# Kernel tuning notes

Hardware: AMD Instinct MI355X
Metric: run time of the kernel (lower is better)

## Reference

```python
import jax, jax.numpy as jnp
import numpy as np

# physics constants (match PDELoss defaults)
RHO, CP, VZ, KT = 0.3, 1200.0, 0.5, 0.06
# Arrhenius-style soot source constants (representative RadiationPINN.soot_source_terms)
A_NUC, E_NUC = 1.0e4, 2.0e4
A_GROW, E_GROW = 5.0e3, 1.2e4
A_OX, E_OX = 1.0e5, 1.6e4

N, IN_DIM, H, OUT, N_FUELS, EMB = 262144, 12, 128, 7, 4, 8


def mlp(X, emb_rows, W1, b1, W2, b2, W3, b3, Wo, bo):
    # X: (N,4) coords; emb_rows: (N,8) fuel embedding -> T (N,1), fv (N,1), Y (N,5)
    h = jnp.concatenate([X, emb_rows], axis=-1)
    h = jnp.tanh(h @ W1 + b1)
    h = jnp.tanh(h @ W2 + b2)
    h = jnp.tanh(h @ W3 + b3)
    o = h @ Wo + bo
    T = 300.0 + 2000.0 * jax.nn.sigmoid(o[:, 0:1])
    fv = jax.nn.softplus(o[:, 1:2]) * 1e-6
    Y = jax.nn.softmax(o[:, 2:7], axis=-1)
    return T, fv, Y


def soot_sources(T, Y_prec, Y_O2, fv):
    nuc = A_NUC * Y_prec * jnp.exp(-E_NUC / T)
    grow = A_GROW * Y_prec * fv * jnp.exp(-E_GROW / T)
    ox = A_OX * Y_O2 * fv * jnp.sqrt(T) * jnp.exp(-E_OX / T)
    return nuc, grow, ox


def pde_loss(inputs, fuel_ids, W1, b1, W2, b2, W3, b3, Wo, bo, emb):
    emb_rows = emb[fuel_ids]  # (N, EMB), constant w.r.t. inputs
    params = (W1, b1, W2, b2, W3, b3, Wo, bo)

    def T_of(X):
        return mlp(X, emb_rows, *params)[0]

    def fv_of(X):
        return mlp(X, emb_rows, *params)[1]

    n = inputs.shape[0]
    Ez = jnp.zeros_like(inputs).at[:, 1].set(1.0)  # direction d/dz
    Er = jnp.zeros_like(inputs).at[:, 2].set(1.0)  # direction d/dr

    # forward-mode (Taylor) derivatives: nested jvp gives 1st and 2nd order in one pass
    dT_dz_fn = lambda X: jax.jvp(T_of, (X,), (Ez,))[1]
    dT_dz, d2T_dz2 = jax.jvp(dT_dz_fn, (inputs,), (Ez,))
    dT_dr_fn = lambda X: jax.jvp(T_of, (X,), (Er,))[1]
    dT_dr, d2T_dr2 = jax.jvp(dT_dr_fn, (inputs,), (Er,))
    _, dfv_dz = jax.jvp(fv_of, (inputs,), (Ez,))

    T, fv, Y = mlp(inputs, emb_rows, *params)
    Y_prec, Y_O2 = Y[:, 3:4], Y[:, 4:5]

    r = inputs[:, 2:3]
    r_safe = jnp.maximum(r, 1e-6)
    laplacian_r = d2T_dr2 + dT_dr / r_safe
    energy_res = RHO * CP * VZ * dT_dz - KT * laplacian_r - KT * d2T_dz2

    nuc, grow, ox = soot_sources(T, Y_prec, Y_O2, fv)
    soot_res = VZ * dfv_dz - nuc - grow + ox

    loss_energy = jnp.mean(energy_res ** 2)
    loss_soot = jnp.mean(soot_res ** 2)
    return jnp.stack([loss_energy, loss_soot, loss_energy + loss_soot])


def setup_inputs() -> dict:
    key = jax.random.key(0)
    ks = jax.random.split(key, 12)
    inputs = jax.random.uniform(ks[0], (N, 4), dtype=jnp.float32)
    fuel_ids = jax.random.randint(ks[1], (N,), 0, N_FUELS)
    s1, sh, so = 1.0 / np.sqrt(IN_DIM), 1.0 / np.sqrt(H), 1.0 / np.sqrt(H)
    return {
        "inputs": inputs,
        "fuel_ids": fuel_ids,
        "W1": jax.random.normal(ks[2], (IN_DIM, H), jnp.float32) * s1,
        "b1": jnp.zeros((H,), jnp.float32),
        "W2": jax.random.normal(ks[3], (H, H), jnp.float32) * sh,
        "b2": jnp.zeros((H,), jnp.float32),
        "W3": jax.random.normal(ks[4], (H, H), jnp.float32) * sh,
        "b3": jnp.zeros((H,), jnp.float32),
        "Wo": jax.random.normal(ks[5], (H, OUT), jnp.float32) * so,
        "bo": jnp.zeros((OUT,), jnp.float32),
        "emb": jax.random.normal(ks[6], (N_FUELS, EMB), jnp.float32) * 0.1,
    }


def reference(inputs, fuel_ids, W1, b1, W2, b2, W3, b3, Wo, bo, emb):
    return pde_loss(inputs, fuel_ids, W1, b1, W2, b2, W3, b3, Wo, bo, emb)
```

## Files before the change

### kernel.cpp

```cpp
#include <hip/hip_runtime.h>
#include <math.h>

#define NPTS 262144
#define PTS  16
#define NBLK (NPTS / PTS)

typedef _Float16 f16;
typedef f16    f16x4 __attribute__((ext_vector_type(4)));
typedef f16    f16x8 __attribute__((ext_vector_type(8)));
typedef __fp16 h16x2 __attribute__((ext_vector_type(2)));
typedef __fp16 h16x4 __attribute__((ext_vector_type(4)));
typedef float  f32x4 __attribute__((ext_vector_type(4)));
typedef int    i32x4 __attribute__((ext_vector_type(4)));


__device__ __forceinline__ h16x2 pk(float a, float b) {
    return __builtin_amdgcn_cvt_pkrtz(a, b);
}
__device__ __forceinline__ f16x4 mrg(h16x2 lo, h16x2 hi) {
    h16x4 v = __builtin_shufflevector(lo, hi, 0, 1, 2, 3);
    return __builtin_bit_cast(f16x4, v);
}
__device__ __forceinline__ int bc(h16x2 v) {
    return __builtin_bit_cast(int, v);
}
__device__ __forceinline__ void pin(f16x8& x) {
    asm volatile("" : "+v"(x));
}

__device__ __forceinline__ float fast_tanh(float z) {
    float e = __expf(2.f * z);
    float r = __builtin_amdgcn_rcpf(e + 1.f);
    return __builtin_fmaf(-2.f, r, 1.f);
}

__global__ void prep_weights(const float* __restrict__ W1, const float* __restrict__ W2,
                             const float* __restrict__ W3, const float* __restrict__ Wo,
                             const float* __restrict__ bo,
                             f16* __restrict__ wt1, f16* __restrict__ wt2,
                             f16* __restrict__ wt3, f16* __restrict__ wot,
                             float* __restrict__ bot)
{
    int tid    = blockIdx.x * blockDim.x + threadIdx.x;
    int stride = gridDim.x * blockDim.x;
    for (int i = tid; i < 128 * 32; i += stride) {
        int k = i >> 7, n = i & 127;
        wt1[n * 32 + k] = (f16)((k < 12) ? W1[k * 128 + n] : 0.f);
    }
    for (int i = tid; i < 128 * 128; i += stride) {
        int k = i >> 7, n = i & 127;
        wt2[n * 128 + k] = (f16)W2[i];
        wt3[n * 128 + k] = (f16)W3[i];
    }
    for (int i = tid; i < 16 * 128; i += stride) {
        int k = i >> 4, n = i & 15;
        wot[n * 128 + k] = (f16)((n < 7) ? Wo[k * 7 + n] : 0.f);
    }
    if (tid < 16) bot[tid] = (tid < 7) ? bo[tid] : 0.f;
}

__device__ __forceinline__ void transform_store(
    char* sA, const f32x4 acc[5], int pt, int n0q)
{
    float t[4], s[4];
#pragma unroll
    for (int r = 0; r < 4; ++r) {
        t[r] = fast_tanh(acc[0][r]);
        s[r] = 1.f - t[r] * t[r];
    }
    h16x2 T[2]  = { pk(t[0], t[1]), pk(t[2], t[3]) };
    h16x2 S[2]  = { pk(s[0], s[1]), pk(s[2], s[3]) };
    h16x2 A1[2] = { pk(acc[1][0], acc[1][1]), pk(acc[1][2], acc[1][3]) };
    h16x2 A2[2] = { pk(acc[2][0], acc[2][1]), pk(acc[2][2], acc[2][3]) };
    h16x2 A3[2] = { pk(acc[3][0], acc[3][1]), pk(acc[3][2], acc[3][3]) };
    h16x2 A4[2] = { pk(acc[4][0], acc[4][1]), pk(acc[4][2], acc[4][3]) };
    h16x2 TZ[2], TZZ[2], TR[2], TRR[2];
#pragma unroll
    for (int p = 0; p < 2; ++p) {
        h16x2 n2t = -(T[p] + T[p]);
        TZ[p]  = S[p] * A1[p];
        TR[p]  = S[p] * A3[p];
        TZZ[p] = n2t * (TZ[p] * A1[p]) + S[p] * A2[p];
        TRR[p] = n2t * (TR[p] * A3[p]) + S[p] * A4[p];
    }
    const int key = (pt & 7) << 4;
    char* rb = sA + (pt << 8) + (((n0q * 2)) ^ key);
    *(f16x4*)(rb)         = mrg(T[0], T[1]);
    *(f16x4*)(rb +  4096) = mrg(TZ[0], TZ[1]);
    *(f16x4*)(rb +  8192) = mrg(TZZ[0], TZZ[1]);
    *(f16x4*)(rb + 12288) = mrg(TR[0], TR[1]);
    *(f16x4*)(rb + 16384) = mrg(TRR[0], TRR[1]);
}

__device__ __forceinline__ void transform_store_l1(
    char* sA, const f32x4 acc0, const f32x4 wz, const f32x4 wr,
    int pt, int n0q)
{
    float t[4], s[4];
#pragma unroll
    for (int r = 0; r < 4; ++r) {
        t[r] = fast_tanh(acc0[r]);
        s[r] = 1.f - t[r] * t[r];
    }
    h16x2 T[2]  = { pk(t[0], t[1]), pk(t[2], t[3]) };
    h16x2 S[2]  = { pk(s[0], s[1]), pk(s[2], s[3]) };
    h16x2 A1[2] = { pk(wz[0], wz[1]), pk(wz[2], wz[3]) };
    h16x2 A3[2] = { pk(wr[0], wr[1]), pk(wr[2], wr[3]) };
    h16x2 TZ[2], TZZ[2], TR[2], TRR[2];
#pragma unroll
    for (int p = 0; p < 2; ++p) {
        h16x2 n2t = -(T[p] + T[p]);
        TZ[p]  = S[p] * A1[p];
        TR[p]  = S[p] * A3[p];
        TZZ[p] = n2t * (TZ[p] * A1[p]);
        TRR[p] = n2t * (TR[p] * A3[p]);
    }
    const int key = (pt & 7) << 4;
    char* rb = sA + (pt << 8) + (((n0q * 2)) ^ key);
    *(f16x4*)(rb)         = mrg(T[0], T[1]);
    *(f16x4*)(rb +  4096) = mrg(TZ[0], TZ[1]);
    *(f16x4*)(rb +  8192) = mrg(TZZ[0], TZZ[1]);
    *(f16x4*)(rb + 12288) = mrg(TR[0], TR[1]);
    *(f16x4*)(rb + 16384) = mrg(TRR[0], TRR[1]);
}

__device__ __forceinline__ void layer128(
    char* sA, const f16* __restrict__ Wt, const float* __restrict__ b,
    int q, int m)
{
    const int mkey = (m & 7) << 4;
    const char* rp = sA + (m << 8);
    f16x8 Bv[5][4];
#pragma unroll
    for (int c = 0; c < 5; ++c)
#pragma unroll
        for (int kt = 0; kt < 4; ++kt) {
            Bv[c][kt] = *(const f16x8*)(rp + c * 4096 + ((kt * 64 + q * 16) ^ mkey));
            pin(Bv[c][kt]);
        }

    const f32x4 z4 = {0.f, 0.f, 0.f, 0.f};
#pragma unroll
    for (int ct0 = 0; ct0 < 8; ++ct0) {
        const int n0 = ct0 * 16;
        const f16* wp = &Wt[(n0 + m) * 128 + q * 8];
        f16x8 A0 = *(const f16x8*)(wp);
        f16x8 A1 = *(const f16x8*)(wp + 32);
        f16x8 A2 = *(const f16x8*)(wp + 64);
        f16x8 A3 = *(const f16x8*)(wp + 96);
        f32x4 bb = *(const f32x4*)&b[n0 + q * 4];
        f32x4 acc[5];
        acc[0] = __builtin_amdgcn_mfma_f32_16x16x32_f16(A0, Bv[0][0], bb, 0, 0, 0);
#pragma unroll
        for (int c = 1; c < 5; ++c) acc[c] = __builtin_amdgcn_mfma_f32_16x16x32_f16(A0, Bv[c][0], z4, 0, 0, 0);
#pragma unroll
        for (int c = 0; c < 5; ++c) acc[c] = __builtin_amdgcn_mfma_f32_16x16x32_f16(A1, Bv[c][1], acc[c], 0, 0, 0);
#pragma unroll
        for (int c = 0; c < 5; ++c) acc[c] = __builtin_amdgcn_mfma_f32_16x16x32_f16(A2, Bv[c][2], acc[c], 0, 0, 0);
#pragma unroll
        for (int c = 0; c < 5; ++c) acc[c] = __builtin_amdgcn_mfma_f32_16x16x32_f16(A3, Bv[c][3], acc[c], 0, 0, 0);

        transform_store(sA, acc, m, n0 + q * 4);
    }
}

__global__ __launch_bounds__(64, 2) void pde_main(
    const float* __restrict__ X,
    const int*   __restrict__ fid,
    const float* __restrict__ emb,
    const float* __restrict__ W1,
    const float* __restrict__ b1, const float* __restrict__ b2,
    const float* __restrict__ b3,
    const f16* __restrict__ Wt1, const f16* __restrict__ Wt2,
    const f16* __restrict__ Wt3, const f16* __restrict__ Wot,
    const float* __restrict__ bot,
    float* __restrict__ partials)
{
    __shared__ f32x4 smem4[1280];
    char* sA = (char*)smem4;

    const int lane = threadIdx.x;
    const int q    = lane >> 4;
    const int m    = lane & 15;
    const int p0   = blockIdx.x * PTS;

    float rcoord = 0.f;
    if (lane < PTS) {
        const int p = lane;
        f32x4 xr = *(const f32x4*)&X[(p0 + p) * 4];
        rcoord = xr.z;
        const float* er = &emb[fid[p0 + p] * 8];
        f32x4 e0 = *(const f32x4*)er;
        f32x4 e1 = *(const f32x4*)(er + 4);
        const int key = (p & 7) << 4;
        char* rb = sA + (p << 8);
        i32x4 w0 = { bc(pk(xr.x, xr.y)), bc(pk(xr.z, xr.w)),
                     bc(pk(e0.x, e0.y)), bc(pk(e0.z, e0.w)) };
        i32x4 w1 = { bc(pk(e1.x, e1.y)), bc(pk(e1.z, e1.w)), 0, 0 };
        const i32x4 z16 = {0, 0, 0, 0};
        *(i32x4*)(rb + (0  ^ key)) = w0;
        *(i32x4*)(rb + (16 ^ key)) = w1;
        *(i32x4*)(rb + (32 ^ key)) = z16;
        *(i32x4*)(rb + (48 ^ key)) = z16;
    }

    {
        const int mkey = (m & 7) << 4;
        f16x8 Bv0 = *(const f16x8*)(sA + (m << 8) + ((q * 16) ^ mkey));
        pin(Bv0);
#pragma unroll
        for (int ct0 = 0; ct0 < 8; ++ct0) {
            const int n0 = ct0 * 16;
            f16x8 A0 = *(const f16x8*)&Wt1[(n0 + m) * 32 + q * 8];
            f32x4 bb = *(const f32x4*)&b1[n0 + q * 4];
            f32x4 acc0 = __builtin_amdgcn_mfma_f32_16x16x32_f16(A0, Bv0, bb, 0, 0, 0);
            f32x4 wz = *(const f32x4*)&W1[128 + n0 + q * 4];
            f32x4 wr = *(const f32x4*)&W1[256 + n0 + q * 4];
            transform_store_l1(sA, acc0, wz, wr, m, n0 + q * 4);
        }
    }

    layer128(sA, Wt2, b2, q, m);
    layer128(sA, Wt3, b3, q, m);

    f32x4 acc[5];
    {
        const int mkey = (m & 7) << 4;
        const char* rp = sA + (m << 8);
        f16x8 Bh[5][4];
#pragma unroll
        for (int c = 0; c < 5; ++c)
#pragma unroll
            for (int kt = 0; kt < 4; ++kt)
                Bh[c][kt] = *(const f16x8*)(rp + c * 4096 + ((kt * 64 + q * 16) ^ mkey));
        f32x4 c0i = *(const f32x4*)&bot[q * 4];
        const f16* wp = &Wot[m * 128 + q * 8];
        f16x8 A0 = *(const f16x8*)(wp);
        f16x8 A1 = *(const f16x8*)(wp + 32);
        f16x8 A2 = *(const f16x8*)(wp + 64);
        f16x8 A3 = *(const f16x8*)(wp + 96);
        const f32x4 z4 = {0.f, 0.f, 0.f, 0.f};
        acc[0] = __builtin_amdgcn_mfma_f32_16x16x32_f16(A0, Bh[0][0], c0i, 0, 0, 0);
#pragma unroll
        for (int c = 1; c < 5; ++c) acc[c] = __builtin_amdgcn_mfma_f32_16x16x32_f16(A0, Bh[c][0], z4, 0, 0, 0);
#pragma unroll
        for (int c = 0; c < 5; ++c) acc[c] = __builtin_amdgcn_mfma_f32_16x16x32_f16(A1, Bh[c][1], acc[c], 0, 0, 0);
#pragma unroll
        for (int c = 0; c < 5; ++c) acc[c] = __builtin_amdgcn_mfma_f32_16x16x32_f16(A2, Bh[c][2], acc[c], 0, 0, 0);
#pragma unroll
        for (int c = 0; c < 5; ++c) acc[c] = __builtin_amdgcn_mfma_f32_16x16x32_f16(A3, Bh[c][3], acc[c], 0, 0, 0);
    }
    const int src = (lane & 15) + 16;
    float o4 = __shfl(acc[0][0], src, 64);
    float o5 = __shfl(acc[0][1], src, 64);
    float o6 = __shfl(acc[0][2], src, 64);

    if (lane < PTS) {
        float o0   = acc[0][0], o1  = acc[0][1];
        float o0z  = acc[1][0], o1z = acc[1][1];
        float o0zz = acc[2][0];
        float o0r  = acc[3][0];
        float o0rr = acc[4][0];

        float sg  = __fdividef(1.f, 1.f + __expf(-o0));
        float T   = 300.f + 2000.f * sg;
        float sp  = sg * (1.f - sg);
        float spp = sp * (1.f - 2.f * sg);
        float Tz  = 2000.f * sp * o0z;
        float Tzz = 2000.f * (spp * o0z * o0z + sp * o0zz);
        float Tr  = 2000.f * sp * o0r;
        float Trr = 2000.f * (spp * o0r * o0r + sp * o0rr);

        float rs  = fmaxf(rcoord, 1e-6f);
        float lap = Trr + __fdividef(Tr, rs);
        float eres = 180.f * Tz - 0.06f * lap - 0.06f * Tzz;

        float fv  = ((o1 > 20.f) ? o1 : __logf(1.f + __expf(o1))) * 1e-6f;
        float s1  = __fdividef(1.f, 1.f + __expf(-o1));
        float fvz = s1 * o1z * 1e-6f;

        float y0 = acc[0][2], y1 = acc[0][3], y2 = o4, y3 = o5, y4 = o6;
        float mx = fmaxf(fmaxf(fmaxf(y0, y1), fmaxf(y2, y3)), y4);
        float e0 = __expf(y0 - mx), e1 = __expf(y1 - mx), e2 = __expf(y2 - mx);
        float e3 = __expf(y3 - mx), e4 = __expf(y4 - mx);
        float inv = __fdividef(1.f, e0 + e1 + e2 + e3 + e4);
        float Yp = e3 * inv;
        float Yo = e4 * inv;

        float rT  = __fdividef(1.f, T);
        float nuc  = 1e4f * Yp * __expf(-20000.f * rT);
        float grow = 5e3f * Yp * fv * __expf(-12000.f * rT);
        float ox   = 1e5f * Yo * fv * sqrtf(T) * __expf(-16000.f * rT);
        float sres = 0.5f * fvz - nuc - grow + ox;

        float ve = eres * eres;
        float vs = sres * sres;
#pragma unroll
        for (int o = 8; o > 0; o >>= 1) {
            ve += __shfl_xor(ve, o, 64);
            vs += __shfl_xor(vs, o, 64);
        }
        if (lane == 0) {
            float2 w; w.x = ve; w.y = vs;
            *(float2*)&partials[2 * blockIdx.x] = w;
        }
    }
}

__global__ __launch_bounds__(1024) void pde_finalize(
    const float* __restrict__ partials, float* __restrict__ out)
{
    __shared__ double rE[1024];
    __shared__ double rS[1024];
    const int tid = threadIdx.x;
    const float2* p2 = (const float2*)partials;
    double se = 0.0, ss = 0.0;
    for (int i = tid; i < NBLK; i += 1024) {
        float2 v = p2[i];
        se += (double)v.x;
        ss += (double)v.y;
    }
    rE[tid] = se; rS[tid] = ss;
    __syncthreads();
    for (int s = 512; s > 0; s >>= 1) {
        if (tid < s) { rE[tid] += rE[tid + s]; rS[tid] += rS[tid + s]; }
        __syncthreads();
    }
    if (tid == 0) {
        const double invN = 1.0 / (double)NPTS;
        float le = (float)(rE[0] * invN);
        float ls = (float)(rS[0] * invN);
        out[0] = le;
        out[1] = ls;
        out[2] = le + ls;
    }
}

extern "C" void kernel_launch(void* const* d_in, const int* in_sizes, int n_in,
                              void* d_out, int out_size, void* d_ws, size_t ws_size,
                              hipStream_t stream)
{
    const float* X   = (const float*)d_in[0];
    const int*   fid = (const int*)  d_in[1];
    const float* W1  = (const float*)d_in[2];
    const float* b1  = (const float*)d_in[3];
    const float* W2  = (const float*)d_in[4];
    const float* b2  = (const float*)d_in[5];
    const float* W3  = (const float*)d_in[6];
    const float* b3  = (const float*)d_in[7];
    const float* Wo  = (const float*)d_in[8];
    const float* bo  = (const float*)d_in[9];
    const float* emb = (const float*)d_in[10];

    f16*   wt1      = (f16*)d_ws;
    f16*   wt2      = wt1 + 128 * 32;
    f16*   wt3      = wt2 + 128 * 128;
    f16*   wot      = wt3 + 128 * 128;
    float* bot      = (float*)(wot + 16 * 128);
    float* partials = bot + 16;
    float* out      = (float*)d_out;

    prep_weights<<<128, 256, 0, stream>>>(W1, W2, W3, Wo, bo, wt1, wt2, wt3, wot, bot);
    pde_main<<<NBLK, 64, 0, stream>>>(X, fid, emb, W1, b1, b2, b3,
                                      wt1, wt2, wt3, wot, bot, partials);
    pde_finalize<<<1, 1024, 0, stream>>>(partials, out);
}
```

Baseline: 239.2 us.

## Keep second-derivative activations in registers via cross-lane shuffle transpose instead of LDS

The TZZ and TRR activation channels are no longer written to shared memory. They are carried in registers and rearranged into the MFMA B-operand layout with wave shuffles (xpose_pair), pairing column tiles. This shrinks LDS from 20KB to 12KB and raises the launch bound to 3 waves per SIMD, to improve occupancy and cut LDS traffic. In exchange it adds many ds_bpermute shuffles and more live registers, which may cause spills under the tighter register budget.

```diff
diff --git a/kernel.cpp b/kernel.cpp
--- a/kernel.cpp
+++ b/kernel.cpp
@@ -24,14 +24,29 @@
 __device__ __forceinline__ int bc(h16x2 v) {
     return __builtin_bit_cast(int, v);
 }
-__device__ __forceinline__ void pin(f16x8& x) {
-    asm volatile("" : "+v"(x));
+__device__ __forceinline__ f16x8 asf16(i32x4 v) {
+    return __builtin_bit_cast(f16x8, v);
 }
 
 __device__ __forceinline__ float fast_tanh(float z) {
     float e = __expf(2.f * z);
     float r = __builtin_amdgcn_rcpf(e + 1.f);
     return __builtin_fmaf(-2.f, r, 1.f);
+}
+
+__device__ __forceinline__ i32x4 xpose_pair(int E0, int E1, int O0, int O1,
+                                            int s0, int s1, int hi)
+{
+    int e0 = __shfl(E0, s0, 64), o0 = __shfl(O0, s0, 64);
+    int e1 = __shfl(E1, s0, 64), o1 = __shfl(O1, s0, 64);
+    int e2 = __shfl(E0, s1, 64), o2 = __shfl(O0, s1, 64);
+    int e3 = __shfl(E1, s1, 64), o3 = __shfl(O1, s1, 64);
+    i32x4 d;
+    d.x = hi ? o0 : e0;
+    d.y = hi ? o1 : e1;
+    d.z = hi ? o2 : e2;
+    d.w = hi ? o3 : e3;
+    return d;
 }
 
 __global__ void prep_weights(const float* __restrict__ W1, const float* __restrict__ W2,
@@ -59,8 +74,9 @@
     if (tid < 16) bot[tid] = (tid < 7) ? bo[tid] : 0.f;
 }
 
-__device__ __forceinline__ void transform_store(
-    char* sA, const f32x4 acc[5], int pt, int n0q)
+__device__ __forceinline__ void transform_store3(
+    char* sA, const f32x4 acc[5], int pt, int n0q,
+    int& zz0, int& zz1, int& rr0, int& rr1)
 {
     float t[4], s[4];
 #pragma unroll
@@ -85,16 +101,16 @@
     }
     const int key = (pt & 7) << 4;
     char* rb = sA + (pt << 8) + (((n0q * 2)) ^ key);
-    *(f16x4*)(rb)         = mrg(T[0], T[1]);
-    *(f16x4*)(rb +  4096) = mrg(TZ[0], TZ[1]);
-    *(f16x4*)(rb +  8192) = mrg(TZZ[0], TZZ[1]);
-    *(f16x4*)(rb + 12288) = mrg(TR[0], TR[1]);
-    *(f16x4*)(rb + 16384) = mrg(TRR[0], TRR[1]);
-}
-
-__device__ __forceinline__ void transform_store_l1(
+    *(f16x4*)(rb)        = mrg(T[0], T[1]);
+    *(f16x4*)(rb + 4096) = mrg(TZ[0], TZ[1]);
+    *(f16x4*)(rb + 8192) = mrg(TR[0], TR[1]);
+    zz0 = bc(TZZ[0]); zz1 = bc(TZZ[1]);
+    rr0 = bc(TRR[0]); rr1 = bc(TRR[1]);
+}
+
+__device__ __forceinline__ void transform_store3_l1(
     char* sA, const f32x4 acc0, const f32x4 wz, const f32x4 wr,
-    int pt, int n0q)
+    int pt, int n0q, int& zz0, int& zz1, int& rr0, int& rr1)
 {
     float t[4], s[4];
 #pragma unroll
@@ -117,54 +133,78 @@
     }
     const int key = (pt & 7) << 4;
     char* rb = sA + (pt << 8) + (((n0q * 2)) ^ key);
-    *(f16x4*)(rb)         = mrg(T[0], T[1]);
-    *(f16x4*)(rb +  4096) = mrg(TZ[0], TZ[1]);
-    *(f16x4*)(rb +  8192) = mrg(TZZ[0], TZZ[1]);
-    *(f16x4*)(rb + 12288) = mrg(TR[0], TR[1]);
-    *(f16x4*)(rb + 16384) = mrg(TRR[0], TRR[1]);
+    *(f16x4*)(rb)        = mrg(T[0], T[1]);
+    *(f16x4*)(rb + 4096) = mrg(TZ[0], TZ[1]);
+    *(f16x4*)(rb + 8192) = mrg(TR[0], TR[1]);
+    zz0 = bc(TZZ[0]); zz1 = bc(TZZ[1]);
+    rr0 = bc(TRR[0]); rr1 = bc(TRR[1]);
 }
 
 __device__ __forceinline__ void layer128(
     char* sA, const f16* __restrict__ Wt, const float* __restrict__ b,
-    int q, int m)
+    int q, int m, int s0, int s1, int hi,
+    const i32x4* Bzz_in, const i32x4* Brr_in,
+    i32x4* Bzz_out, i32x4* Brr_out)
 {
     const int mkey = (m & 7) << 4;
     const char* rp = sA + (m << 8);
-    f16x8 Bv[5][4];
-#pragma unroll
-    for (int c = 0; c < 5; ++c)
-#pragma unroll
-        for (int kt = 0; kt < 4; ++kt) {
+    f16x8 Bv[3][4];
+#pragma unroll
+    for (int c = 0; c < 3; ++c)
+#pragma unroll
+        for (int kt = 0; kt < 4; ++kt)
             Bv[c][kt] = *(const f16x8*)(rp + c * 4096 + ((kt * 64 + q * 16) ^ mkey));
-            pin(Bv[c][kt]);
+
+    const f32x4 z4 = {0.f, 0.f, 0.f, 0.f};
+#pragma unroll
+    for (int pr = 0; pr < 4; ++pr) {
+        int zE0, zE1, rE0, rE1, zO0, zO1, rO0, rO1;
+#pragma unroll
+        for (int half = 0; half < 2; ++half) {
+            const int ct0 = pr * 2 + half;
+            const int n0 = ct0 * 16;
+            const f16* wp = &Wt[(n0 + m) * 128 + q * 8];
+            f16x8 A0 = *(const f16x8*)(wp);
+            f16x8 A1 = *(const f16x8*)(wp + 32);
+            f16x8 A2 = *(const f16x8*)(wp + 64);
+            f16x8 A3 = *(const f16x8*)(wp + 96);
+            f32x4 bb = *(const f32x4*)&b[n0 + q * 4];
+            f32x4 acc[5];
+            acc[0] = __builtin_amdgcn_mfma_f32_16x16x32_f16(A0, Bv[0][0], bb, 0, 0, 0);
+            acc[1] = __builtin_amdgcn_mfma_f32_16x16x32_f16(A0, Bv[1][0], z4, 0, 0, 0);
+            acc[2] = __builtin_amdgcn_mfma_f32_16x16x32_f16(A0, asf16(Bzz_in[0]), z4, 0, 0, 0);
+            acc[3] = __builtin_amdgcn_mfma_f32_16x16x32_f16(A0, Bv[2][0], z4, 0, 0, 0);
+            acc[4] = __builtin_amdgcn_mfma_f32_16x16x32_f16(A0, asf16(Brr_in[0]), z4, 0, 0, 0);
+
+            acc[0] = __builtin_amdgcn_mfma_f32_16x16x32_f16(A1, Bv[0][1], acc[0], 0, 0, 0);
+            acc[1] = __builtin_amdgcn_mfma_f32_16x16x32_f16(A1, Bv[1][1], acc[1], 0, 0, 0);
+            acc[2] = __builtin_amdgcn_mfma_f32_16x16x32_f16(A1, asf16(Bzz_in[1]), acc[2], 0, 0, 0);
+            acc[3] = __builtin_amdgcn_mfma_f32_16x16x32_f16(A1, Bv[2][1], acc[3], 0, 0, 0);
+            acc[4] = __builtin_amdgcn_mfma_f32_16x16x32_f16(A1, asf16(Brr_in[1]), acc[4], 0, 0, 0);
+
+            acc[0] = __builtin_amdgcn_mfma_f32_16x16x32_f16(A2, Bv[0][2], acc[0], 0, 0, 0);
+            acc[1] = __builtin_amdgcn_mfma_f32_16x16x32_f16(A2, Bv[1][2], acc[1], 0, 0, 0);
+            acc[2] = __builtin_amdgcn_mfma_f32_16x16x32_f16(A2, asf16(Bzz_in[2]), acc[2], 0, 0, 0);
+            acc[3] = __builtin_amdgcn_mfma_f32_16x16x32_f16(A2, Bv[2][2], acc[3], 0, 0, 0);
+            acc[4] = __builtin_amdgcn_mfma_f32_16x16x32_f16(A2, asf16(Brr_in[2]), acc[4], 0, 0, 0);
+
+            acc[0] = __builtin_amdgcn_mfma_f32_16x16x32_f16(A3, Bv[0][3], acc[0], 0, 0, 0);
+            acc[1] = __builtin_amdgcn_mfma_f32_16x16x32_f16(A3, Bv[1][3], acc[1], 0, 0, 0);
+            acc[2] = __builtin_amdgcn_mfma_f32_16x16x32_f16(A3, asf16(Bzz_in[3]), acc[2], 0, 0, 0);
+            acc[3] = __builtin_amdgcn_mfma_f32_16x16x32_f16(A3, Bv[2][3], acc[3], 0, 0, 0);
+            acc[4] = __builtin_amdgcn_mfma_f32_16x16x32_f16(A3, asf16(Brr_in[3]), acc[4], 0, 0, 0);
+
+            int z0, z1, r0, r1;
+            transform_store3(sA, acc, m, n0 + q * 4, z0, z1, r0, r1);
+            if (half == 0) { zE0 = z0; zE1 = z1; rE0 = r0; rE1 = r1; }
+            else           { zO0 = z0; zO1 = z1; rO0 = r0; rO1 = r1; }
         }
-
-    const f32x4 z4 = {0.f, 0.f, 0.f, 0.f};
-#pragma unroll
-    for (int ct0 = 0; ct0 < 8; ++ct0) {
-        const int n0 = ct0 * 16;
-        const f16* wp = &Wt[(n0 + m) * 128 + q * 8];
-        f16x8 A0 = *(const f16x8*)(wp);
-        f16x8 A1 = *(const f16x8*)(wp + 32);
-        f16x8 A2 = *(const f16x8*)(wp + 64);
-        f16x8 A3 = *(const f16x8*)(wp + 96);
-        f32x4 bb = *(const f32x4*)&b[n0 + q * 4];
-        f32x4 acc[5];
-        acc[0] = __builtin_amdgcn_mfma_f32_16x16x32_f16(A0, Bv[0][0], bb, 0, 0, 0);
-#pragma unroll
-        for (int c = 1; c < 5; ++c) acc[c] = __builtin_amdgcn_mfma_f32_16x16x32_f16(A0, Bv[c][0], z4, 0, 0, 0);
-#pragma unroll
-        for (int c = 0; c < 5; ++c) acc[c] = __builtin_amdgcn_mfma_f32_16x16x32_f16(A1, Bv[c][1], acc[c], 0, 0, 0);
-#pragma unroll
-        for (int c = 0; c < 5; ++c) acc[c] = __builtin_amdgcn_mfma_f32_16x16x32_f16(A2, Bv[c][2], acc[c], 0, 0, 0);
-#pragma unroll
-        for (int c = 0; c < 5; ++c) acc[c] = __builtin_amdgcn_mfma_f32_16x16x32_f16(A3, Bv[c][3], acc[c], 0, 0, 0);
-
-        transform_store(sA, acc, m, n0 + q * 4);
-    }
-}
-
-__global__ __launch_bounds__(64, 2) void pde_main(
+        Bzz_out[pr] = xpose_pair(zE0, zE1, zO0, zO1, s0, s1, hi);
+        Brr_out[pr] = xpose_pair(rE0, rE1, rO0, rO1, s0, s1, hi);
+    }
+}
+
+__global__ __launch_bounds__(64, 3) void pde_main(
     const float* __restrict__ X,
     const int*   __restrict__ fid,
     const float* __restrict__ emb,
@@ -176,13 +216,16 @@
     const float* __restrict__ bot,
     float* __restrict__ partials)
 {
-    __shared__ f32x4 smem4[1280];
+    __shared__ f32x4 smem4[768];
     char* sA = (char*)smem4;
 
     const int lane = threadIdx.x;
     const int q    = lane >> 4;
     const int m    = lane & 15;
     const int p0   = blockIdx.x * PTS;
+    const int s0   = ((q & 1) << 5) + m;
+    const int s1   = s0 + 16;
+    const int hi   = q >> 1;
 
     float rcoord = 0.f;
     if (lane < PTS) {
@@ -204,32 +247,43 @@
         *(i32x4*)(rb + (48 ^ key)) = z16;
     }
 
+    i32x4 BzzA[4], BrrA[4], BzzB[4], BrrB[4];
+
     {
         const int mkey = (m & 7) << 4;
         f16x8 Bv0 = *(const f16x8*)(sA + (m << 8) + ((q * 16) ^ mkey));
-        pin(Bv0);
-#pragma unroll
-        for (int ct0 = 0; ct0 < 8; ++ct0) {
-            const int n0 = ct0 * 16;
-            f16x8 A0 = *(const f16x8*)&Wt1[(n0 + m) * 32 + q * 8];
-            f32x4 bb = *(const f32x4*)&b1[n0 + q * 4];
-            f32x4 acc0 = __builtin_amdgcn_mfma_f32_16x16x32_f16(A0, Bv0, bb, 0, 0, 0);
-            f32x4 wz = *(const f32x4*)&W1[128 + n0 + q * 4];
-            f32x4 wr = *(const f32x4*)&W1[256 + n0 + q * 4];
-            transform_store_l1(sA, acc0, wz, wr, m, n0 + q * 4);
+#pragma unroll
+        for (int pr = 0; pr < 4; ++pr) {
+            int zE0, zE1, rE0, rE1, zO0, zO1, rO0, rO1;
+#pragma unroll
+            for (int half = 0; half < 2; ++half) {
+                const int ct0 = pr * 2 + half;
+                const int n0 = ct0 * 16;
+                f16x8 A0 = *(const f16x8*)&Wt1[(n0 + m) * 32 + q * 8];
+                f32x4 bb = *(const f32x4*)&b1[n0 + q * 4];
+                f32x4 acc0 = __builtin_amdgcn_mfma_f32_16x16x32_f16(A0, Bv0, bb, 0, 0, 0);
+                f32x4 wz = *(const f32x4*)&W1[128 + n0 + q * 4];
+                f32x4 wr = *(const f32x4*)&W1[256 + n0 + q * 4];
+                int z0, z1, r0, r1;
+                transform_store3_l1(sA, acc0, wz, wr, m, n0 + q * 4, z0, z1, r0, r1);
+                if (half == 0) { zE0 = z0; zE1 = z1; rE0 = r0; rE1 = r1; }
+                else           { zO0 = z0; zO1 = z1; rO0 = r0; rO1 = r1; }
+            }
+            BzzA[pr] = xpose_pair(zE0, zE1, zO0, zO1, s0, s1, hi);
+            BrrA[pr] = xpose_pair(rE0, rE1, rO0, rO1, s0, s1, hi);
         }
     }
 
-    layer128(sA, Wt2, b2, q, m);
-    layer128(sA, Wt3, b3, q, m);
+    layer128(sA, Wt2, b2, q, m, s0, s1, hi, BzzA, BrrA, BzzB, BrrB);
+    layer128(sA, Wt3, b3, q, m, s0, s1, hi, BzzB, BrrB, BzzA, BrrA);
 
     f32x4 acc[5];
     {
         const int mkey = (m & 7) << 4;
         const char* rp = sA + (m << 8);
-        f16x8 Bh[5][4];
-#pragma unroll
-        for (int c = 0; c < 5; ++c)
+        f16x8 Bh[3][4];
+#pragma unroll
+        for (int c = 0; c < 3; ++c)
 #pragma unroll
             for (int kt = 0; kt < 4; ++kt)
                 Bh[c][kt] = *(const f16x8*)(rp + c * 4096 + ((kt * 64 + q * 16) ^ mkey));
@@ -241,14 +295,28 @@
         f16x8 A3 = *(const f16x8*)(wp + 96);
         const f32x4 z4 = {0.f, 0.f, 0.f, 0.f};
         acc[0] = __builtin_amdgcn_mfma_f32_16x16x32_f16(A0, Bh[0][0], c0i, 0, 0, 0);
-#pragma unroll
-        for (int c = 1; c < 5; ++c) acc[c] = __builtin_amdgcn_mfma_f32_16x16x32_f16(A0, Bh[c][0], z4, 0, 0, 0);
-#pragma unroll
-        for (int c = 0; c < 5; ++c) acc[c] = __builtin_amdgcn_mfma_f32_16x16x32_f16(A1, Bh[c][1], acc[c], 0, 0, 0);
-#pragma unroll
-        for (int c = 0; c < 5; ++c) acc[c] = __builtin_amdgcn_mfma_f32_16x16x32_f16(A2, Bh[c][2], acc[c], 0, 0, 0);
-#pragma unroll
-        for (int c = 0; c < 5; ++c) acc[c] = __builtin_amdgcn_mfma_f32_16x16x32_f16(A3, Bh[c][3], acc[c], 0, 0, 0);
+        acc[1] = __builtin_amdgcn_mfma_f32_16x16x32_f16(A0, Bh[1][0], z4, 0, 0, 0);
+        acc[2] = __builtin_amdgcn_mfma_f32_16x16x32_f16(A0, asf16(BzzA[0]), z4, 0, 0, 0);
+        acc[3] = __builtin_amdgcn_mfma_f32_16x16x32_f16(A0, Bh[2][0], z4, 0, 0, 0);
+        acc[4] = __builtin_amdgcn_mfma_f32_16x16x32_f16(A0, asf16(BrrA[0]), z4, 0, 0, 0);
+
+        acc[0] = __builtin_amdgcn_mfma_f32_16x16x32_f16(A1, Bh[0][1], acc[0], 0, 0, 0);
+        acc[1] = __builtin_amdgcn_mfma_f32_16x16x32_f16(A1, Bh[1][1], acc[1], 0, 0, 0);
+        acc[2] = __builtin_amdgcn_mfma_f32_16x16x32_f16(A1, asf16(BzzA[1]), acc[2], 0, 0, 0);
+        acc[3] = __builtin_amdgcn_mfma_f32_16x16x32_f16(A1, Bh[2][1], acc[3], 0, 0, 0);
+        acc[4] = __builtin_amdgcn_mfma_f32_16x16x32_f16(A1, asf16(BrrA[1]), acc[4], 0, 0, 0);
+
+        acc[0] = __builtin_amdgcn_mfma_f32_16x16x32_f16(A2, Bh[0][2], acc[0], 0, 0, 0);
+        acc[1] = __builtin_amdgcn_mfma_f32_16x16x32_f16(A2, Bh[1][2], acc[1], 0, 0, 0);
+        acc[2] = __builtin_amdgcn_mfma_f32_16x16x32_f16(A2, asf16(BzzA[2]), acc[2], 0, 0, 0);
+        acc[3] = __builtin_amdgcn_mfma_f32_16x16x32_f16(A2, Bh[2][2], acc[3], 0, 0, 0);
+        acc[4] = __builtin_amdgcn_mfma_f32_16x16x32_f16(A2, asf16(BrrA[2]), acc[4], 0, 0, 0);
+
+        acc[0] = __builtin_amdgcn_mfma_f32_16x16x32_f16(A3, Bh[0][3], acc[0], 0, 0, 0);
+        acc[1] = __builtin_amdgcn_mfma_f32_16x16x32_f16(A3, Bh[1][3], acc[1], 0, 0, 0);
+        acc[2] = __builtin_amdgcn_mfma_f32_16x16x32_f16(A3, asf16(BzzA[3]), acc[2], 0, 0, 0);
+        acc[3] = __builtin_amdgcn_mfma_f32_16x16x32_f16(A3, Bh[2][3], acc[3], 0, 0, 0);
+        acc[4] = __builtin_amdgcn_mfma_f32_16x16x32_f16(A3, asf16(BrrA[3]), acc[4], 0, 0, 0);
     }
     const int src = (lane & 15) + 16;
     float o4 = __shfl(acc[0][0], src, 64);
@@ -276,8 +344,8 @@
         float eres = 180.f * Tz - 0.06f * lap - 0.06f * Tzz;
 
         float fv  = ((o1 > 20.f) ? o1 : __logf(1.f + __expf(o1))) * 1e-6f;
-        float s1  = __fdividef(1.f, 1.f + __expf(-o1));
-        float fvz = s1 * o1z * 1e-6f;
+        float s1v = __fdividef(1.f, 1.f + __expf(-o1));
+        float fvz = s1v * o1z * 1e-6f;
 
         float y0 = acc[0][2], y1 = acc[0][3], y2 = o4, y3 = o5, y4 = o6;
         float mx = fmaxf(fmaxf(fmaxf(y0, y1), fmaxf(y2, y3)), y4);
```

After: 239.6 us. About the same (+0.1%).

## Switch MLP tiles to 32x32x16 MFMA with 32 points per block

Applied to the files above, without the earlier changes.

Each wavefront now processes 32 points and uses 32x32x16 MFMA instructions instead of 16x16x32, so each weight A-fragment load is reused across 32 points and more work goes through each matrix instruction. The LDS activation layout, swizzle key, first-layer and output weight padding, and the reduction width are all rewritten to match. Each layer keeps five 16-wide accumulators and 40 B-fragments live, which raises register pressure. Occupancy is cut to one wave per launch-bounds hint and LDS doubles to 40KB, which risks less latency hiding.

```diff
diff --git a/kernel.cpp b/kernel.cpp
--- a/kernel.cpp
+++ b/kernel.cpp
@@ -2,7 +2,7 @@
 #include <math.h>
 
 #define NPTS 262144
-#define PTS  16
+#define PTS  32
 #define NBLK (NPTS / PTS)
 
 typedef _Float16 f16;
@@ -11,6 +11,7 @@
 typedef __fp16 h16x2 __attribute__((ext_vector_type(2)));
 typedef __fp16 h16x4 __attribute__((ext_vector_type(4)));
 typedef float  f32x4 __attribute__((ext_vector_type(4)));
+typedef float  f32x16 __attribute__((ext_vector_type(16)));
 typedef int    i32x4 __attribute__((ext_vector_type(4)));
 
 
@@ -24,8 +25,11 @@
 __device__ __forceinline__ int bc(h16x2 v) {
     return __builtin_bit_cast(int, v);
 }
-__device__ __forceinline__ void pin(f16x8& x) {
-    asm volatile("" : "+v"(x));
+__device__ __forceinline__ f32x16 zero16() {
+    f32x16 z;
+#pragma unroll
+    for (int i = 0; i < 16; ++i) z[i] = 0.f;
+    return z;
 }
 
 __device__ __forceinline__ float fast_tanh(float z) {
@@ -43,37 +47,38 @@
 {
     int tid    = blockIdx.x * blockDim.x + threadIdx.x;
     int stride = gridDim.x * blockDim.x;
-    for (int i = tid; i < 128 * 32; i += stride) {
-        int k = i >> 7, n = i & 127;
-        wt1[n * 32 + k] = (f16)((k < 12) ? W1[k * 128 + n] : 0.f);
+    for (int i = tid; i < 128 * 16; i += stride) {
+        int k = i & 15, n = i >> 4;
+        wt1[n * 16 + k] = (f16)((k < 12) ? W1[k * 128 + n] : 0.f);
     }
     for (int i = tid; i < 128 * 128; i += stride) {
         int k = i >> 7, n = i & 127;
         wt2[n * 128 + k] = (f16)W2[i];
         wt3[n * 128 + k] = (f16)W3[i];
     }
-    for (int i = tid; i < 16 * 128; i += stride) {
-        int k = i >> 4, n = i & 15;
+    for (int i = tid; i < 32 * 128; i += stride) {
+        int k = i >> 5, n = i & 31;
         wot[n * 128 + k] = (f16)((n < 7) ? Wo[k * 7 + n] : 0.f);
     }
-    if (tid < 16) bot[tid] = (tid < 7) ? bo[tid] : 0.f;
-}
-
-__device__ __forceinline__ void transform_store(
-    char* sA, const f32x4 acc[5], int pt, int n0q)
+    if (tid < 32) bot[tid] = (tid < 7) ? bo[tid] : 0.f;
+}
+
+__device__ __forceinline__ void transform_store4(
+    char* sA, const f32x4 a0v, const f32x4 a1v, const f32x4 a2v,
+    const f32x4 a3v, const f32x4 a4v, int pt, int n)
 {
     float t[4], s[4];
 #pragma unroll
     for (int r = 0; r < 4; ++r) {
-        t[r] = fast_tanh(acc[0][r]);
+        t[r] = fast_tanh(a0v[r]);
         s[r] = 1.f - t[r] * t[r];
     }
     h16x2 T[2]  = { pk(t[0], t[1]), pk(t[2], t[3]) };
     h16x2 S[2]  = { pk(s[0], s[1]), pk(s[2], s[3]) };
-    h16x2 A1[2] = { pk(acc[1][0], acc[1][1]), pk(acc[1][2], acc[1][3]) };
-    h16x2 A2[2] = { pk(acc[2][0], acc[2][1]), pk(acc[2][2], acc[2][3]) };
-    h16x2 A3[2] = { pk(acc[3][0], acc[3][1]), pk(acc[3][2], acc[3][3]) };
-    h16x2 A4[2] = { pk(acc[4][0], acc[4][1]), pk(acc[4][2], acc[4][3]) };
+    h16x2 A1[2] = { pk(a1v[0], a1v[1]), pk(a1v[2], a1v[3]) };
+    h16x2 A2[2] = { pk(a2v[0], a2v[1]), pk(a2v[2], a2v[3]) };
+    h16x2 A3[2] = { pk(a3v[0], a3v[1]), pk(a3v[2], a3v[3]) };
+    h16x2 A4[2] = { pk(a4v[0], a4v[1]), pk(a4v[2], a4v[3]) };
     h16x2 TZ[2], TZZ[2], TR[2], TRR[2];
 #pragma unroll
     for (int p = 0; p < 2; ++p) {
@@ -83,23 +88,22 @@
         TZZ[p] = n2t * (TZ[p] * A1[p]) + S[p] * A2[p];
         TRR[p] = n2t * (TR[p] * A3[p]) + S[p] * A4[p];
     }
-    const int key = (pt & 7) << 4;
-    char* rb = sA + (pt << 8) + (((n0q * 2)) ^ key);
+    const int key = (pt & 15) << 4;
+    char* rb = sA + (pt << 8) + ((n * 2) ^ key);
     *(f16x4*)(rb)         = mrg(T[0], T[1]);
-    *(f16x4*)(rb +  4096) = mrg(TZ[0], TZ[1]);
-    *(f16x4*)(rb +  8192) = mrg(TZZ[0], TZZ[1]);
-    *(f16x4*)(rb + 12288) = mrg(TR[0], TR[1]);
-    *(f16x4*)(rb + 16384) = mrg(TRR[0], TRR[1]);
-}
-
-__device__ __forceinline__ void transform_store_l1(
-    char* sA, const f32x4 acc0, const f32x4 wz, const f32x4 wr,
-    int pt, int n0q)
+    *(f16x4*)(rb +  8192) = mrg(TZ[0], TZ[1]);
+    *(f16x4*)(rb + 16384) = mrg(TZZ[0], TZZ[1]);
+    *(f16x4*)(rb + 24576) = mrg(TR[0], TR[1]);
+    *(f16x4*)(rb + 32768) = mrg(TRR[0], TRR[1]);
+}
+
+__device__ __forceinline__ void transform_store4_l1(
+    char* sA, const f32x4 a0v, const f32x4 wz, const f32x4 wr, int pt, int n)
 {
     float t[4], s[4];
 #pragma unroll
     for (int r = 0; r < 4; ++r) {
-        t[r] = fast_tanh(acc0[r]);
+        t[r] = fast_tanh(a0v[r]);
         s[r] = 1.f - t[r] * t[r];
     }
     h16x2 T[2]  = { pk(t[0], t[1]), pk(t[2], t[3]) };
@@ -115,56 +119,61 @@
         TZZ[p] = n2t * (TZ[p] * A1[p]);
         TRR[p] = n2t * (TR[p] * A3[p]);
     }
-    const int key = (pt & 7) << 4;
-    char* rb = sA + (pt << 8) + (((n0q * 2)) ^ key);
+    const int key = (pt & 15) << 4;
+    char* rb = sA + (pt << 8) + ((n * 2) ^ key);
     *(f16x4*)(rb)         = mrg(T[0], T[1]);
-    *(f16x4*)(rb +  4096) = mrg(TZ[0], TZ[1]);
-    *(f16x4*)(rb +  8192) = mrg(TZZ[0], TZZ[1]);
-    *(f16x4*)(rb + 12288) = mrg(TR[0], TR[1]);
-    *(f16x4*)(rb + 16384) = mrg(TRR[0], TRR[1]);
-}
-
-__device__ __forceinline__ void layer128(
+    *(f16x4*)(rb +  8192) = mrg(TZ[0], TZ[1]);
+    *(f16x4*)(rb + 16384) = mrg(TZZ[0], TZZ[1]);
+    *(f16x4*)(rb + 24576) = mrg(TR[0], TR[1]);
+    *(f16x4*)(rb + 32768) = mrg(TRR[0], TRR[1]);
+}
+
+__device__ __forceinline__ void layer128w(
     char* sA, const f16* __restrict__ Wt, const float* __restrict__ b,
-    int q, int m)
-{
-    const int mkey = (m & 7) << 4;
-    const char* rp = sA + (m << 8);
-    f16x8 Bv[5][4];
+    int col, int hi, int key)
+{
+    const char* rp = sA + (col << 8);
+    f16x8 Bv[5][8];
 #pragma unroll
     for (int c = 0; c < 5; ++c)
 #pragma unroll
-        for (int kt = 0; kt < 4; ++kt) {
-            Bv[c][kt] = *(const f16x8*)(rp + c * 4096 + ((kt * 64 + q * 16) ^ mkey));
-            pin(Bv[c][kt]);
-        }
-
-    const f32x4 z4 = {0.f, 0.f, 0.f, 0.f};
-#pragma unroll
-    for (int ct0 = 0; ct0 < 8; ++ct0) {
-        const int n0 = ct0 * 16;
-        const f16* wp = &Wt[(n0 + m) * 128 + q * 8];
-        f16x8 A0 = *(const f16x8*)(wp);
-        f16x8 A1 = *(const f16x8*)(wp + 32);
-        f16x8 A2 = *(const f16x8*)(wp + 64);
-        f16x8 A3 = *(const f16x8*)(wp + 96);
-        f32x4 bb = *(const f32x4*)&b[n0 + q * 4];
-        f32x4 acc[5];
-        acc[0] = __builtin_amdgcn_mfma_f32_16x16x32_f16(A0, Bv[0][0], bb, 0, 0, 0);
-#pragma unroll
-        for (int c = 1; c < 5; ++c) acc[c] = __builtin_amdgcn_mfma_f32_16x16x32_f16(A0, Bv[c][0], z4, 0, 0, 0);
-#pragma unroll
-        for (int c = 0; c < 5; ++c) acc[c] = __builtin_amdgcn_mfma_f32_16x16x32_f16(A1, Bv[c][1], acc[c], 0, 0, 0);
-#pragma unroll
-        for (int c = 0; c < 5; ++c) acc[c] = __builtin_amdgcn_mfma_f32_16x16x32_f16(A2, Bv[c][2], acc[c], 0, 0, 0);
-#pragma unroll
-        for (int c = 0; c < 5; ++c) acc[c] = __builtin_amdgcn_mfma_f32_16x16x32_f16(A3, Bv[c][3], acc[c], 0, 0, 0);
-
-        transform_store(sA, acc, m, n0 + q * 4);
-    }
-}
-
-__global__ __launch_bounds__(64, 2) void pde_main(
+        for (int ks = 0; ks < 8; ++ks)
+            Bv[c][ks] = *(const f16x8*)(rp + c * 8192 + ((ks * 32 + hi * 16) ^ key));
+
+#pragma unroll
+    for (int ct0 = 0; ct0 < 4; ++ct0) {
+        const int n0 = ct0 * 32;
+        f32x16 acc0;
+#pragma unroll
+        for (int rg = 0; rg < 4; ++rg) {
+            f32x4 bv = *(const f32x4*)&b[n0 + rg * 8 + hi * 4];
+            acc0[rg * 4 + 0] = bv[0]; acc0[rg * 4 + 1] = bv[1];
+            acc0[rg * 4 + 2] = bv[2]; acc0[rg * 4 + 3] = bv[3];
+        }
+        f32x16 acc1 = zero16(), acc2 = zero16(), acc3 = zero16(), acc4 = zero16();
+#pragma unroll
+        for (int ks = 0; ks < 8; ++ks) {
+            f16x8 A = *(const f16x8*)&Wt[(n0 + col) * 128 + ks * 16 + hi * 8];
+            acc0 = __builtin_amdgcn_mfma_f32_32x32x16_f16(A, Bv[0][ks], acc0, 0, 0, 0);
+            acc1 = __builtin_amdgcn_mfma_f32_32x32x16_f16(A, Bv[1][ks], acc1, 0, 0, 0);
+            acc2 = __builtin_amdgcn_mfma_f32_32x32x16_f16(A, Bv[2][ks], acc2, 0, 0, 0);
+            acc3 = __builtin_amdgcn_mfma_f32_32x32x16_f16(A, Bv[3][ks], acc3, 0, 0, 0);
+            acc4 = __builtin_amdgcn_mfma_f32_32x32x16_f16(A, Bv[4][ks], acc4, 0, 0, 0);
+        }
+#pragma unroll
+        for (int rg = 0; rg < 4; ++rg) {
+            const int nb = n0 + rg * 8 + hi * 4;
+            f32x4 s0 = {acc0[rg*4], acc0[rg*4+1], acc0[rg*4+2], acc0[rg*4+3]};
+            f32x4 s1 = {acc1[rg*4], acc1[rg*4+1], acc1[rg*4+2], acc1[rg*4+3]};
+            f32x4 s2 = {acc2[rg*4], acc2[rg*4+1], acc2[rg*4+2], acc2[rg*4+3]};
+            f32x4 s3 = {acc3[rg*4], acc3[rg*4+1], acc3[rg*4+2], acc3[rg*4+3]};
+            f32x4 s4 = {acc4[rg*4], acc4[rg*4+1], acc4[rg*4+2], acc4[rg*4+3]};
+            transform_store4(sA, s0, s1, s2, s3, s4, col, nb);
+        }
+    }
+}
+
+__global__ __launch_bounds__(64, 1) void pde_main(
     const float* __restrict__ X,
     const int*   __restrict__ fid,
     const float* __restrict__ emb,
@@ -176,91 +185,96 @@
     const float* __restrict__ bot,
     float* __restrict__ partials)
 {
-    __shared__ f32x4 smem4[1280];
+    __shared__ f32x4 smem4[2560];
     char* sA = (char*)smem4;
 
     const int lane = threadIdx.x;
-    const int q    = lane >> 4;
-    const int m    = lane & 15;
+    const int col  = lane & 31;
+    const int hi   = lane >> 5;
+    const int key  = (col & 15) << 4;
     const int p0   = blockIdx.x * PTS;
 
     float rcoord = 0.f;
     if (lane < PTS) {
-        const int p = lane;
-        f32x4 xr = *(const f32x4*)&X[(p0 + p) * 4];
+        const int p = p0 + lane;
+        f32x4 xr = *(const f32x4*)&X[p * 4];
         rcoord = xr.z;
-        const float* er = &emb[fid[p0 + p] * 8];
+        const float* er = &emb[fid[p] * 8];
         f32x4 e0 = *(const f32x4*)er;
         f32x4 e1 = *(const f32x4*)(er + 4);
-        const int key = (p & 7) << 4;
-        char* rb = sA + (p << 8);
+        char* rb = sA + (col << 8);
         i32x4 w0 = { bc(pk(xr.x, xr.y)), bc(pk(xr.z, xr.w)),
                      bc(pk(e0.x, e0.y)), bc(pk(e0.z, e0.w)) };
         i32x4 w1 = { bc(pk(e1.x, e1.y)), bc(pk(e1.z, e1.w)), 0, 0 };
-        const i32x4 z16 = {0, 0, 0, 0};
         *(i32x4*)(rb + (0  ^ key)) = w0;
         *(i32x4*)(rb + (16 ^ key)) = w1;
-        *(i32x4*)(rb + (32 ^ key)) = z16;
-        *(i32x4*)(rb + (48 ^ key)) = z16;
     }
 
     {
-        const int mkey = (m & 7) << 4;
-        f16x8 Bv0 = *(const f16x8*)(sA + (m << 8) + ((q * 16) ^ mkey));
-        pin(Bv0);
-#pragma unroll
-        for (int ct0 = 0; ct0 < 8; ++ct0) {
-            const int n0 = ct0 * 16;
-            f16x8 A0 = *(const f16x8*)&Wt1[(n0 + m) * 32 + q * 8];
-            f32x4 bb = *(const f32x4*)&b1[n0 + q * 4];
-            f32x4 acc0 = __builtin_amdgcn_mfma_f32_16x16x32_f16(A0, Bv0, bb, 0, 0, 0);
-            f32x4 wz = *(const f32x4*)&W1[128 + n0 + q * 4];
-            f32x4 wr = *(const f32x4*)&W1[256 + n0 + q * 4];
-            transform_store_l1(sA, acc0, wz, wr, m, n0 + q * 4);
-        }
-    }
-
-    layer128(sA, Wt2, b2, q, m);
-    layer128(sA, Wt3, b3, q, m);
-
-    f32x4 acc[5];
+        f16x8 Bv0 = *(const f16x8*)(sA + (col << 8) + ((hi * 16) ^ key));
+#pragma unroll
+        for (int ct0 = 0; ct0 < 4; ++ct0) {
+            const int n0 = ct0 * 32;
+            f16x8 A0 = *(const f16x8*)&Wt1[(n0 + col) * 16 + hi * 8];
+            f32x16 acc0;
+#pragma unroll
+            for (int rg = 0; rg < 4; ++rg) {
+                f32x4 bv = *(const f32x4*)&b1[n0 + rg * 8 + hi * 4];
+                acc0[rg * 4 + 0] = bv[0]; acc0[rg * 4 + 1] = bv[1];
+                acc0[rg * 4 + 2] = bv[2]; acc0[rg * 4 + 3] = bv[3];
+            }
+            acc0 = __builtin_amdgcn_mfma_f32_32x32x16_f16(A0, Bv0, acc0, 0, 0, 0);
+#pragma unroll
+            for (int rg = 0; rg < 4; ++rg) {
+                const int nb = n0 + rg * 8 + hi * 4;
+                f32x4 a0 = {acc0[rg*4], acc0[rg*4+1], acc0[rg*4+2], acc0[rg*4+3]};
+                f32x4 wz = *(const f32x4*)&W1[128 + nb];
+                f32x4 wr = *(const f32x4*)&W1[256 + nb];
+                transform_store4_l1(sA, a0, wz, wr, col, nb);
+            }
+        }
+    }
+
+    layer128w(sA, Wt2, b2, col, hi, key);
+    layer128w(sA, Wt3, b3, col, hi, key);
+
+    f32x16 h0, h1, h2, h3, h4;
     {
-        const int mkey = (m & 7) << 4;
-        const char* rp = sA + (m << 8);
-        f16x8 Bh[5][4];
+        const char* rp = sA + (col << 8);
+        f16x8 Bh[5][8];
 #pragma unroll
         for (int c = 0; c < 5; ++c)
 #pragma unroll
-            for (int kt = 0; kt < 4; ++kt)
-                Bh[c][kt] = *(const f16x8*)(rp + c * 4096 + ((kt * 64 + q * 16) ^ mkey));
-        f32x4 c0i = *(const f32x4*)&bot[q * 4];
-        const f16* wp = &Wot[m * 128 + q * 8];
-        f16x8 A0 = *(const f16x8*)(wp);
-        f16x8 A1 = *(const f16x8*)(wp + 32);
-        f16x8 A2 = *(const f16x8*)(wp + 64);
-        f16x8 A3 = *(const f16x8*)(wp + 96);
-        const f32x4 z4 = {0.f, 0.f, 0.f, 0.f};
-        acc[0] = __builtin_amdgcn_mfma_f32_16x16x32_f16(A0, Bh[0][0], c0i, 0, 0, 0);
-#pragma unroll
-        for (int c = 1; c < 5; ++c) acc[c] = __builtin_amdgcn_mfma_f32_16x16x32_f16(A0, Bh[c][0], z4, 0, 0, 0);
-#pragma unroll
-        for (int c = 0; c < 5; ++c) acc[c] = __builtin_amdgcn_mfma_f32_16x16x32_f16(A1, Bh[c][1], acc[c], 0, 0, 0);
-#pragma unroll
-        for (int c = 0; c < 5; ++c) acc[c] = __builtin_amdgcn_mfma_f32_16x16x32_f16(A2, Bh[c][2], acc[c], 0, 0, 0);
-#pragma unroll
-        for (int c = 0; c < 5; ++c) acc[c] = __builtin_amdgcn_mfma_f32_16x16x32_f16(A3, Bh[c][3], acc[c], 0, 0, 0);
-    }
-    const int src = (lane & 15) + 16;
-    float o4 = __shfl(acc[0][0], src, 64);
-    float o5 = __shfl(acc[0][1], src, 64);
-    float o6 = __shfl(acc[0][2], src, 64);
+            for (int ks = 0; ks < 8; ++ks)
+                Bh[c][ks] = *(const f16x8*)(rp + c * 8192 + ((ks * 32 + hi * 16) ^ key));
+#pragma unroll
+        for (int rg = 0; rg < 4; ++rg) {
+            f32x4 bv = *(const f32x4*)&bot[rg * 8 + hi * 4];
+            h0[rg * 4 + 0] = bv[0]; h0[rg * 4 + 1] = bv[1];
+            h0[rg * 4 + 2] = bv[2]; h0[rg * 4 + 3] = bv[3];
+        }
+        h1 = zero16(); h2 = zero16(); h3 = zero16(); h4 = zero16();
+#pragma unroll
+        for (int ks = 0; ks < 8; ++ks) {
+            f16x8 A = *(const f16x8*)&Wot[col * 128 + ks * 16 + hi * 8];
+            h0 = __builtin_amdgcn_mfma_f32_32x32x16_f16(A, Bh[0][ks], h0, 0, 0, 0);
+            h1 = __builtin_amdgcn_mfma_f32_32x32x16_f16(A, Bh[1][ks], h1, 0, 0, 0);
+            h2 = __builtin_amdgcn_mfma_f32_32x32x16_f16(A, Bh[2][ks], h2, 0, 0, 0);
+            h3 = __builtin_amdgcn_mfma_f32_32x32x16_f16(A, Bh[3][ks], h3, 0, 0, 0);
+            h4 = __builtin_amdgcn_mfma_f32_32x32x16_f16(A, Bh[4][ks], h4, 0, 0, 0);
+        }
+    }
+    const int src = col + 32;
+    float o4 = __shfl(h0[0], src, 64);
+    float o5 = __shfl(h0[1], src, 64);
+    float o6 = __shfl(h0[2], src, 64);
 
     if (lane < PTS) {
-        float o0   = acc[0][0], o1  = acc[0][1];
-        float o0z  = acc[1][0], o1z = acc[1][1];
-        float o0zz = acc[2][0];
-        float o0r  = acc[3][0];
-        float o0rr = acc[4][0];
+        float o0   = h0[0], o1  = h0[1];
+        float o0z  = h1[0], o1z = h1[1];
+        float o0zz = h2[0];
+        float o0r  = h3[0];
+        float o0rr = h4[0];
 
         float sg  = __fdividef(1.f, 1.f + __expf(-o0));
         float T   = 300.f + 2000.f * sg;
@@ -276,10 +290,10 @@
         float eres = 180.f * Tz - 0.06f * lap - 0.06f * Tzz;
 
         float fv  = ((o1 > 20.f) ? o1 : __logf(1.f + __expf(o1))) * 1e-6f;
-        float s1  = __fdividef(1.f, 1.f + __expf(-o1));
-        float fvz = s1 * o1z * 1e-6f;
-
-        float y0 = acc[0][2], y1 = acc[0][3], y2 = o4, y3 = o5, y4 = o6;
+        float s1v = __fdividef(1.f, 1.f + __expf(-o1));
+        float fvz = s1v * o1z * 1e-6f;
+
+        float y0 = h0[2], y1 = h0[3], y2 = o4, y3 = o5, y4 = o6;
         float mx = fmaxf(fmaxf(fmaxf(y0, y1), fmaxf(y2, y3)), y4);
         float e0 = __expf(y0 - mx), e1 = __expf(y1 - mx), e2 = __expf(y2 - mx);
         float e3 = __expf(y3 - mx), e4 = __expf(y4 - mx);
@@ -296,7 +310,7 @@
         float ve = eres * eres;
         float vs = sres * sres;
 #pragma unroll
-        for (int o = 8; o > 0; o >>= 1) {
+        for (int o = 16; o > 0; o >>= 1) {
             ve += __shfl_xor(ve, o, 64);
             vs += __shfl_xor(vs, o, 64);
         }
@@ -353,11 +367,11 @@
     const float* emb = (const float*)d_in[10];
 
     f16*   wt1      = (f16*)d_ws;
-    f16*   wt2      = wt1 + 128 * 32;
+    f16*   wt2      = wt1 + 128 * 16;
     f16*   wt3      = wt2 + 128 * 128;
     f16*   wot      = wt3 + 128 * 128;
-    float* bot      = (float*)(wot + 16 * 128);
-    float* partials = bot + 16;
+    float* bot      = (float*)(wot + 32 * 128);
+    float* partials = bot + 32;
     float* out      = (float*)d_out;
 
     prep_weights<<<128, 256, 0, stream>>>(W1, W2, W3, Wo, bo, wt1, wt2, wt3, wot, bot);
```

New measurement: 261.5 us. 1.09x slower.
